# Optimization experiments

Measured on AMD Instinct MI355X. Metric: run time of the kernel, lower is better.

Reference implementation:

```python
import jax, jax.numpy as jnp
import numpy as np
from jax.scipy.special import gammaln

EPSILON = 1e-8
BOHR2ANG = 0.529177249  # Angstrom per Bohr; vecs are converted Ang -> Bohr
LS = np.array([0, 0, 0, 0, 1, 1, 1, 2, 2])             # angular momentum per orbital (9 GTOs, Lmax=2)
RAD_IDX = np.repeat(np.arange(len(LS)), 2 * LS + 1)    # [23] orbital index for each (orbital, m) slot
SPH_IDX = np.concatenate([np.arange(l * l, l * l + 2 * l + 1) for l in LS])  # [23] index into flat SH (dim 9)
OUTDIM = len(RAD_IDX)                                  # 23
BSZ, NPROBE, NATOM = 8, 8000, 32


def sph_harm_norm(u):
    """Real spherical harmonics l=0..2 of unit vectors u, e3nn 'norm' normalization (||Y_l||=1).
    Component-normalized e3nn polynomials divided by sqrt(2l+1). [..., 3] -> [..., 9]."""
    x, y, z = u[..., 0], u[..., 1], u[..., 2]
    s3 = 1.7320508075688772  # sqrt(3)
    sh = [
        jnp.ones_like(x),                       # l=0
        x, y, z,                                # l=1: sqrt(3)*(x,y,z)/sqrt(3)
        s3 * x * z,                             # l=2 (component / sqrt(5))
        s3 * x * y,
        y * y - 0.5 * (x * x + z * z),
        s3 * y * z,
        0.5 * s3 * (z * z - x * x),
    ]
    return jnp.stack(sh, axis=-1)


def _pair_indices(n_probes, n_atoms):
    """Host-side ragged atom-probe pair index construction (same result as the torch offset math)."""
    npb, naa = np.asarray(n_probes), np.asarray(n_atoms)
    offs_p, offs_a = np.cumsum(npb) - npb, np.cumsum(naa) - naa
    ip, ia = [], []
    for b in range(len(npb)):  # loop over small batch of molecules only
        ip.append(np.repeat(np.arange(npb[b]) + offs_p[b], naa[b]))
        ia.append(np.tile(np.arange(naa[b]) + offs_a[b], npb[b]))
    return jnp.asarray(np.concatenate(ip)), jnp.asarray(np.concatenate(ia))


def _gto(vecs, expos, ls):
    """GTOs.compute with normalize=True, expo_scaling=None. vecs: [P,3] (Bohr)."""
    r = jnp.linalg.norm(vecs, axis=-1, keepdims=True) + EPSILON   # [P,1]
    sph = sph_harm_norm(vecs / r)                                  # [P,9]
    power = ls + 1.5
    lognorm = (power * jnp.log(2.0 * expos) + jnp.log(2.0) - gammaln(power)) * 0.5  # [9]
    radial = jnp.exp(-expos * (r * r) + ls * jnp.log(r) + lognorm)  # [P,9]
    return radial[:, RAD_IDX] * sph[:, SPH_IDX]                     # [P,23] uncontracted


def setup_inputs() -> dict:
    key = jax.random.key(0)
    k1, k2, k3, k4 = jax.random.split(key, 4)
    probe_coords = jax.random.uniform(k1, (BSZ * NPROBE, 3), minval=0.0, maxval=10.0)
    atom_coords = jax.random.uniform(k2, (BSZ * NATOM, 3), minval=0.0, maxval=10.0)
    coeffs = 0.1 * jax.random.normal(k3, (BSZ * NATOM, OUTDIM))
    expos = jax.random.uniform(k4, (len(LS),), minval=0.2, maxval=5.0)
    n_probes = jnp.full((BSZ,), NPROBE, dtype=jnp.int32)
    n_atoms = jnp.full((BSZ,), NATOM, dtype=jnp.int32)
    return {"probe_coords": probe_coords, "atom_coords": atom_coords,
            "n_probes": n_probes, "n_atoms": n_atoms, "coeffs": coeffs, "expos": expos}


def reference(probe_coords, atom_coords, n_probes, n_atoms, coeffs, expos):
    ip, ia = _pair_indices(n_probes, n_atoms)           # [P] each, P = sum(n_probes*n_atoms)
    vecs = probe_coords[ip] - atom_coords[ia]           # [P,3]
    vecs = vecs[:, [1, 2, 0]] / BOHR2ANG                # reorder=True, Ang -> Bohr
    ls = jnp.asarray(LS, dtype=vecs.dtype)
    unc = _gto(vecs, expos, ls)                         # [P,23]
    per_pair = jnp.sum(unc * coeffs[ia], axis=-1)       # [P]
    n_total_probes = int(np.asarray(n_probes).sum())
    return jax.ops.segment_sum(per_pair, ip, num_segments=n_total_probes)  # [n_total_probes]
```

## Files before the change

### kernel.cpp

```cpp
#include <hip/hip_runtime.h>
#include <hip/hip_bf16.h>

#define SUB 4

__global__ __launch_bounds__(256) void gto_kernel(
    const float* __restrict__ probe,
    const float* __restrict__ atom,
    const int* __restrict__ n_probes,
    const int* __restrict__ n_atoms,
    const float* __restrict__ coeffs,
    const float* __restrict__ expos,
    float* __restrict__ out,
    int bsz, int ptot)
{
    const int t = blockIdx.x * blockDim.x + threadIdx.x;
    const int p = t / SUB;
    const int sub = t % SUB;
    if (p >= ptot) return;

    int poff = 0, aoff = 0, na = 0;
    for (int b = 0; b < bsz; ++b) {
        int np = n_probes[b];
        int nb = n_atoms[b];
        if (p < poff + np) { na = nb; break; }
        poff += np; aoff += nb;
    }

    const float gl[3] = {-0.12078223763524522f, 0.28468287047291918f, 1.2009736023470742f};
    const int   lsq[9] = {0,0,0,0,1,1,1,2,2};
    float e[9], ln[9];
#pragma unroll
    for (int k = 0; k < 9; ++k) {
        e[k] = expos[k];
        float pw = (float)lsq[k] + 1.5f;
        ln[k] = 0.5f * (pw * __logf(2.0f * e[k]) + 0.69314718055994531f - gl[lsq[k]]);
    }

    const float INV_BOHR = 1.8897259885789233f;
    const float S3 = 1.7320508075688772f;

    const float px = probe[p * 3 + 0];
    const float py = probe[p * 3 + 1];
    const float pz = probe[p * 3 + 2];

    float acc = 0.0f;
    for (int a = sub; a < na; a += SUB) {
        const int ai = aoff + a;
        const float ax = atom[ai * 3 + 0];
        const float ay = atom[ai * 3 + 1];
        const float az = atom[ai * 3 + 2];

        const float x = (py - ay) * INV_BOHR;
        const float y = (pz - az) * INV_BOHR;
        const float z = (px - ax) * INV_BOHR;

        const float r2n = x * x + y * y + z * z;
        const float r   = sqrtf(r2n) + 1e-8f;
        const float inv = 1.0f / r;
        const float ux = x * inv, uy = y * inv, uz = z * inv;
        const float rr = r * r;

        float rad[9];
#pragma unroll
        for (int k = 0; k < 9; ++k) rad[k] = __expf(ln[k] - e[k] * rr);
        rad[4] *= r;  rad[5] *= r;  rad[6] *= r;
        rad[7] *= rr; rad[8] *= rr;

        const float sh4 = S3 * ux * uz;
        const float sh5 = S3 * ux * uy;
        const float sh6 = uy * uy - 0.5f * (ux * ux + uz * uz);
        const float sh7 = S3 * uy * uz;
        const float sh8 = 0.5f * S3 * (uz * uz - ux * ux);

        const float* c = coeffs + ai * 23;
        float pp;
        pp  = rad[0] * c[0] + rad[1] * c[1] + rad[2] * c[2] + rad[3] * c[3];
        pp += rad[4] * (ux * c[4]  + uy * c[5]  + uz * c[6]);
        pp += rad[5] * (ux * c[7]  + uy * c[8]  + uz * c[9]);
        pp += rad[6] * (ux * c[10] + uy * c[11] + uz * c[12]);
        pp += rad[7] * (sh4 * c[13] + sh5 * c[14] + sh6 * c[15] + sh7 * c[16] + sh8 * c[17]);
        pp += rad[8] * (sh4 * c[18] + sh5 * c[19] + sh6 * c[20] + sh7 * c[21] + sh8 * c[22]);
        acc += pp;
    }

#pragma unroll
    for (int ofs = SUB / 2; ofs > 0; ofs >>= 1)
        acc += __shfl_xor(acc, ofs, 64);

    if (sub == 0) out[p] = acc;
}

extern "C" void kernel_launch(void* const* d_in, const int* in_sizes, int n_in,
                              void* d_out, int out_size, void* d_ws, size_t ws_size,
                              hipStream_t stream) {
    const float* probe  = (const float*)d_in[0];
    const float* atom   = (const float*)d_in[1];
    const int*   n_prb  = (const int*)d_in[2];
    const int*   n_atm  = (const int*)d_in[3];
    const float* coeffs = (const float*)d_in[4];
    const float* expos  = (const float*)d_in[5];
    float*       out    = (float*)d_out;

    const int bsz  = in_sizes[2];
    const int ptot = out_size;

    const int threads = ptot * SUB;
    const int block = 256;
    const int grid = (threads + block - 1) / block;
    gto_kernel<<<grid, block, 0, stream>>>(probe, atom, n_prb, n_atm, coeffs, expos, out, bsz, ptot);
}
```

Measured before the change: 17.21 us.

## Prepack scaled atom coefficients and drop sqrt/divide from GTO inner loop

Adds a pre-pass kernel that writes each atom into a 28-float workspace row holding its Bohr-scaled coordinates and its coefficients pre-multiplied by the radial normalisation and spherical-harmonic constants. The main kernel then reads each row as seven float4 loads. It removes sqrt, reciprocal and the r^l factors by using the unnormalised polynomial forms, and computes the exponentials with exp2. The cost is a second kernel launch and a small workspace write. Dropping the 1e-8 epsilon on r slightly changes numerics near r=0.

```diff
diff --git a/kernel.cpp b/kernel.cpp
--- a/kernel.cpp
+++ b/kernel.cpp
@@ -2,14 +2,51 @@
 #include <hip/hip_bf16.h>
 
 #define SUB 4
+#define ROWF 28
+
+__device__ __constant__ int   kRadIdx[23] = {0,1,2,3, 4,4,4, 5,5,5, 6,6,6, 7,7,7,7,7, 8,8,8,8,8};
+
+__global__ __launch_bounds__(256) void pack_kernel(
+    const float* __restrict__ atom,
+    const float* __restrict__ coeffs,
+    const float* __restrict__ expos,
+    float* __restrict__ ws,
+    int atot)
+{
+    const int a = blockIdx.x * blockDim.x + threadIdx.x;
+    if (a >= atot) return;
+
+    const float gl[3]  = {-0.12078223763524522f, 0.28468287047291918f, 1.2009736023470742f};
+    const int   lsq[9] = {0,0,0,0,1,1,1,2,2};
+    const float S3 = 1.7320508075688772f;
+    const float shf[23] = {1,1,1,1, 1,1,1, 1,1,1, 1,1,1,
+                           S3, S3, 1.0f, S3, 0.5f*S3,
+                           S3, S3, 1.0f, S3, 0.5f*S3};
+    float en[9];
+#pragma unroll
+    for (int k = 0; k < 9; ++k) {
+        float e  = expos[k];
+        float pw = (float)lsq[k] + 1.5f;
+        float ln = 0.5f * (pw * __logf(2.0f * e) + 0.69314718055994531f - gl[lsq[k]]);
+        en[k] = __expf(ln);
+    }
+    const float IB = 1.8897259885789233f;
+    float* row = ws + a * ROWF;
+    row[0] = atom[a * 3 + 1] * IB;
+    row[1] = atom[a * 3 + 2] * IB;
+    row[2] = atom[a * 3 + 0] * IB;
+#pragma unroll
+    for (int s = 0; s < 23; ++s)
+        row[3 + s] = coeffs[a * 23 + s] * en[kRadIdx[s]] * shf[s];
+    row[26] = 0.0f; row[27] = 0.0f;
+}
 
 __global__ __launch_bounds__(256) void gto_kernel(
     const float* __restrict__ probe,
-    const float* __restrict__ atom,
     const int* __restrict__ n_probes,
     const int* __restrict__ n_atoms,
-    const float* __restrict__ coeffs,
     const float* __restrict__ expos,
+    const float* __restrict__ ws,
     float* __restrict__ out,
     int bsz, int ptot)
 {
@@ -26,60 +63,45 @@
         poff += np; aoff += nb;
     }
 
-    const float gl[3] = {-0.12078223763524522f, 0.28468287047291918f, 1.2009736023470742f};
-    const int   lsq[9] = {0,0,0,0,1,1,1,2,2};
-    float e[9], ln[9];
+    const float NL2 = -1.4426950408889634f;
+    float e2n[9];
 #pragma unroll
-    for (int k = 0; k < 9; ++k) {
-        e[k] = expos[k];
-        float pw = (float)lsq[k] + 1.5f;
-        ln[k] = 0.5f * (pw * __logf(2.0f * e[k]) + 0.69314718055994531f - gl[lsq[k]]);
-    }
+    for (int k = 0; k < 9; ++k) e2n[k] = expos[k] * NL2;
 
-    const float INV_BOHR = 1.8897259885789233f;
-    const float S3 = 1.7320508075688772f;
-
-    const float px = probe[p * 3 + 0];
-    const float py = probe[p * 3 + 1];
-    const float pz = probe[p * 3 + 2];
+    const float IB = 1.8897259885789233f;
+    const float pxs = probe[p * 3 + 1] * IB;
+    const float pys = probe[p * 3 + 2] * IB;
+    const float pzs = probe[p * 3 + 0] * IB;
 
     float acc = 0.0f;
     for (int a = sub; a < na; a += SUB) {
-        const int ai = aoff + a;
-        const float ax = atom[ai * 3 + 0];
-        const float ay = atom[ai * 3 + 1];
-        const float az = atom[ai * 3 + 2];
+        const float4* row = (const float4*)(ws + (size_t)(aoff + a) * ROWF);
+        const float4 f0 = row[0], f1 = row[1], f2 = row[2], f3 = row[3];
+        const float4 f4 = row[4], f5 = row[5], f6 = row[6];
 
-        const float x = (py - ay) * INV_BOHR;
-        const float y = (pz - az) * INV_BOHR;
-        const float z = (px - ax) * INV_BOHR;
+        const float x = pxs - f0.x;
+        const float y = pys - f0.y;
+        const float z = pzs - f0.z;
+        const float xx = x * x, yy = y * y, zz = z * z;
+        const float r2 = xx + yy + zz;
 
-        const float r2n = x * x + y * y + z * z;
-        const float r   = sqrtf(r2n) + 1e-8f;
-        const float inv = 1.0f / r;
-        const float ux = x * inv, uy = y * inv, uz = z * inv;
-        const float rr = r * r;
+        float er[9];
+#pragma unroll
+        for (int k = 0; k < 9; ++k) er[k] = __builtin_amdgcn_exp2f(e2n[k] * r2);
 
-        float rad[9];
-#pragma unroll
-        for (int k = 0; k < 9; ++k) rad[k] = __expf(ln[k] - e[k] * rr);
-        rad[4] *= r;  rad[5] *= r;  rad[6] *= r;
-        rad[7] *= rr; rad[8] *= rr;
+        const float q1 = x * z;
+        const float q2 = x * y;
+        const float q4 = y * z;
+        const float q3 = yy - 0.5f * (xx + zz);
+        const float q5 = zz - xx;
 
-        const float sh4 = S3 * ux * uz;
-        const float sh5 = S3 * ux * uy;
-        const float sh6 = uy * uy - 0.5f * (ux * ux + uz * uz);
-        const float sh7 = S3 * uy * uz;
-        const float sh8 = 0.5f * S3 * (uz * uz - ux * ux);
-
-        const float* c = coeffs + ai * 23;
         float pp;
-        pp  = rad[0] * c[0] + rad[1] * c[1] + rad[2] * c[2] + rad[3] * c[3];
-        pp += rad[4] * (ux * c[4]  + uy * c[5]  + uz * c[6]);
-        pp += rad[5] * (ux * c[7]  + uy * c[8]  + uz * c[9]);
-        pp += rad[6] * (ux * c[10] + uy * c[11] + uz * c[12]);
-        pp += rad[7] * (sh4 * c[13] + sh5 * c[14] + sh6 * c[15] + sh7 * c[16] + sh8 * c[17]);
-        pp += rad[8] * (sh4 * c[18] + sh5 * c[19] + sh6 * c[20] + sh7 * c[21] + sh8 * c[22]);
+        pp  = er[0] * f0.w + er[1] * f1.x + er[2] * f1.y + er[3] * f1.z;
+        pp += er[4] * (x * f1.w + y * f2.x + z * f2.y);
+        pp += er[5] * (x * f2.z + y * f2.w + z * f3.x);
+        pp += er[6] * (x * f3.y + y * f3.z + z * f3.w);
+        pp += er[7] * (q1 * f4.x + q2 * f4.y + q3 * f4.z + q4 * f4.w + q5 * f5.x);
+        pp += er[8] * (q1 * f5.y + q2 * f5.z + q3 * f5.w + q4 * f6.x + q5 * f6.y);
         acc += pp;
     }
 
@@ -100,12 +122,16 @@
     const float* coeffs = (const float*)d_in[4];
     const float* expos  = (const float*)d_in[5];
     float*       out    = (float*)d_out;
+    float*       ws     = (float*)d_ws;
 
     const int bsz  = in_sizes[2];
+    const int atot = in_sizes[1] / 3;
     const int ptot = out_size;
+
+    pack_kernel<<<(atot + 255) / 256, 256, 0, stream>>>(atom, coeffs, expos, ws, atot);
 
     const int threads = ptot * SUB;
     const int block = 256;
     const int grid = (threads + block - 1) / block;
-    gto_kernel<<<grid, block, 0, stream>>>(probe, atom, n_prb, n_atm, coeffs, expos, out, bsz, ptot);
+    gto_kernel<<<grid, block, 0, stream>>>(probe, n_prb, n_atm, expos, ws, out, bsz, ptot);
 }
```

After: 21.31 us. 1.24x slower.

## Fold radial powers into unnormalized harmonics, use exp2, vectorize coefficient loads

Applied to the files above, without the earlier changes.

Uses the algebraic identity r^l * Y_l(u) = polynomial in x,y,z, which removes the sqrt, the reciprocal and the per-l radial multiplies. Switches to native exp2 with log2-domain normalization constants, prescales probe coordinates so each difference is a single fma, and loads the coefficients as vectors. It also replaces the batch lookup with a wave-shuffle broadcast and keeps out-of-range lanes alive for the shuffle reduction. This drops the 1e-8 epsilon on r, which slightly changes numerics near r=0, and the unaligned vector loads rely on 4-byte alignment.

```diff
diff --git a/kernel.cpp b/kernel.cpp
--- a/kernel.cpp
+++ b/kernel.cpp
@@ -1,7 +1,9 @@
 #include <hip/hip_runtime.h>
-#include <hip/hip_bf16.h>
 
 #define SUB 4
+
+typedef float f4u __attribute__((ext_vector_type(4), aligned(4)));
+typedef float f2u __attribute__((ext_vector_type(2), aligned(4)));
 
 __global__ __launch_bounds__(256) void gto_kernel(
     const float* __restrict__ probe,
@@ -14,80 +16,108 @@
     int bsz, int ptot)
 {
     const int t = blockIdx.x * blockDim.x + threadIdx.x;
-    const int p = t / SUB;
-    const int sub = t % SUB;
-    if (p >= ptot) return;
+    int p = t / SUB;
+    const int sub = t & (SUB - 1);
+    const bool alive = (p < ptot);
+    if (!alive) p = ptot - 1;
+    const int lane = threadIdx.x & 63;
 
-    int poff = 0, aoff = 0, na = 0;
-    for (int b = 0; b < bsz; ++b) {
-        int np = n_probes[b];
-        int nb = n_atoms[b];
-        if (p < poff + np) { na = nb; break; }
-        poff += np; aoff += nb;
+    int aoff = 0, na = 0;
+    if (bsz <= 64) {
+        int npl = 0, nal = 0;
+        if (lane < bsz) { npl = n_probes[lane]; nal = n_atoms[lane]; }
+        int cp = 0, ca = 0;
+        for (int b = 0; b < bsz; ++b) {
+            const int np_b = __shfl(npl, b, 64);
+            const int na_b = __shfl(nal, b, 64);
+            if (p >= cp && p < cp + np_b) { aoff = ca; na = na_b; }
+            cp += np_b; ca += na_b;
+        }
+    } else {
+        int cp = 0, ca = 0;
+        for (int b = 0; b < bsz; ++b) {
+            const int np_b = n_probes[b];
+            const int na_b = n_atoms[b];
+            if (p >= cp && p < cp + np_b) { aoff = ca; na = na_b; }
+            cp += np_b; ca += na_b;
+        }
     }
 
-    const float gl[3] = {-0.12078223763524522f, 0.28468287047291918f, 1.2009736023470742f};
-    const int   lsq[9] = {0,0,0,0,1,1,1,2,2};
-    float e[9], ln[9];
+    const float gl2[3]  = {-0.17425190f, 0.41071060f, 1.73263870f};
+    const int   lsq[9]  = {0,0,0,0,1,1,1,2,2};
+    const float NL2 = -1.4426950408889634f;
+    float e2n[9], lb2[9];
 #pragma unroll
     for (int k = 0; k < 9; ++k) {
-        e[k] = expos[k];
-        float pw = (float)lsq[k] + 1.5f;
-        ln[k] = 0.5f * (pw * __logf(2.0f * e[k]) + 0.69314718055994531f - gl[lsq[k]]);
+        const float e  = expos[k];
+        const float pw = (float)lsq[k] + 1.5f;
+        e2n[k] = e * NL2;
+        lb2[k] = 0.5f * (pw * __log2f(2.0f * e) + 1.0f - gl2[lsq[k]]);
     }
 
-    const float INV_BOHR = 1.8897259885789233f;
-    const float S3 = 1.7320508075688772f;
+    const float IB  = 1.8897259885789233f;
+    const float S3  = 1.7320508075688772f;
+    const float HS3 = 0.8660254037844386f;
 
-    const float px = probe[p * 3 + 0];
-    const float py = probe[p * 3 + 1];
-    const float pz = probe[p * 3 + 2];
+    const float pxs = probe[p * 3 + 1] * IB;
+    const float pys = probe[p * 3 + 2] * IB;
+    const float pzs = probe[p * 3 + 0] * IB;
 
     float acc = 0.0f;
+#pragma unroll 2
     for (int a = sub; a < na; a += SUB) {
-        const int ai = aoff + a;
-        const float ax = atom[ai * 3 + 0];
-        const float ay = atom[ai * 3 + 1];
-        const float az = atom[ai * 3 + 2];
+        const size_t ai = (size_t)(aoff + a);
+        const float* ar = atom + ai * 3;
+        const float a0 = ar[0], a1 = ar[1], a2 = ar[2];
+        const float* cr = coeffs + ai * 23;
+        const f4u c0 = *(const f4u*)(cr);
+        const f4u c4 = *(const f4u*)(cr + 4);
+        const f4u c8 = *(const f4u*)(cr + 8);
+        const f4u cc = *(const f4u*)(cr + 12);
+        const f4u cg = *(const f4u*)(cr + 16);
+        const f2u ck = *(const f2u*)(cr + 20);
+        const float cm = cr[22];
 
-        const float x = (py - ay) * INV_BOHR;
-        const float y = (pz - az) * INV_BOHR;
-        const float z = (px - ax) * INV_BOHR;
+        const float x = __builtin_fmaf(-IB, a1, pxs);
+        const float y = __builtin_fmaf(-IB, a2, pys);
+        const float z = __builtin_fmaf(-IB, a0, pzs);
+        const float xx = x * x, yy = y * y, zz = z * z;
+        const float r2 = xx + yy + zz;
 
-        const float r2n = x * x + y * y + z * z;
-        const float r   = sqrtf(r2n) + 1e-8f;
-        const float inv = 1.0f / r;
-        const float ux = x * inv, uy = y * inv, uz = z * inv;
-        const float rr = r * r;
+        float er[9];
+#pragma unroll
+        for (int k = 0; k < 9; ++k)
+            er[k] = __builtin_amdgcn_exp2f(__builtin_fmaf(e2n[k], r2, lb2[k]));
 
-        float rad[9];
-#pragma unroll
-        for (int k = 0; k < 9; ++k) rad[k] = __expf(ln[k] - e[k] * rr);
-        rad[4] *= r;  rad[5] *= r;  rad[6] *= r;
-        rad[7] *= rr; rad[8] *= rr;
-
-        const float sh4 = S3 * ux * uz;
-        const float sh5 = S3 * ux * uy;
-        const float sh6 = uy * uy - 0.5f * (ux * ux + uz * uz);
-        const float sh7 = S3 * uy * uz;
-        const float sh8 = 0.5f * S3 * (uz * uz - ux * ux);
-
-        const float* c = coeffs + ai * 23;
-        float pp;
-        pp  = rad[0] * c[0] + rad[1] * c[1] + rad[2] * c[2] + rad[3] * c[3];
-        pp += rad[4] * (ux * c[4]  + uy * c[5]  + uz * c[6]);
-        pp += rad[5] * (ux * c[7]  + uy * c[8]  + uz * c[9]);
-        pp += rad[6] * (ux * c[10] + uy * c[11] + uz * c[12]);
-        pp += rad[7] * (sh4 * c[13] + sh5 * c[14] + sh6 * c[15] + sh7 * c[16] + sh8 * c[17]);
-        pp += rad[8] * (sh4 * c[18] + sh5 * c[19] + sh6 * c[20] + sh7 * c[21] + sh8 * c[22]);
-        acc += pp;
+        float s = er[0] * c0.x;
+        s = __builtin_fmaf(er[1], c0.y, s);
+        s = __builtin_fmaf(er[2], c0.z, s);
+        s = __builtin_fmaf(er[3], c0.w, s);
+        float d;
+        d = __builtin_fmaf(x, c4.x, __builtin_fmaf(y, c4.y, z * c4.z));
+        s = __builtin_fmaf(er[4], d, s);
+        d = __builtin_fmaf(x, c4.w, __builtin_fmaf(y, c8.x, z * c8.y));
+        s = __builtin_fmaf(er[5], d, s);
+        d = __builtin_fmaf(x, c8.z, __builtin_fmaf(y, c8.w, z * cc.x));
+        s = __builtin_fmaf(er[6], d, s);
+        const float u1 = S3 * (x * z);
+        const float u2 = S3 * (x * y);
+        const float q3 = __builtin_fmaf(-0.5f, xx + zz, yy);
+        const float u4 = S3 * (y * z);
+        const float u5 = HS3 * (zz - xx);
+        d = __builtin_fmaf(u1, cc.y, __builtin_fmaf(u2, cc.z,
+            __builtin_fmaf(q3, cc.w, __builtin_fmaf(u4, cg.x, u5 * cg.y))));
+        s = __builtin_fmaf(er[7], d, s);
+        d = __builtin_fmaf(u1, cg.z, __builtin_fmaf(u2, cg.w,
+            __builtin_fmaf(q3, ck.x, __builtin_fmaf(u4, ck.y, u5 * cm))));
+        s = __builtin_fmaf(er[8], d, s);
+        acc += s;
     }
 
-#pragma unroll
-    for (int ofs = SUB / 2; ofs > 0; ofs >>= 1)
-        acc += __shfl_xor(acc, ofs, 64);
+    acc += __shfl_xor(acc, 1, 64);
+    acc += __shfl_xor(acc, 2, 64);
 
-    if (sub == 0) out[p] = acc;
+    if (alive && sub == 0) out[p] = acc;
 }
 
 extern "C" void kernel_launch(void* const* d_in, const int* in_sizes, int n_in,
@@ -104,8 +134,8 @@
     const int bsz  = in_sizes[2];
     const int ptot = out_size;
 
-    const int threads = ptot * SUB;
+    const long threads = (long)ptot * SUB;
     const int block = 256;
-    const int grid = (threads + block - 1) / block;
+    const int grid = (int)((threads + block - 1) / block);
     gto_kernel<<<grid, block, 0, stream>>>(probe, atom, n_prb, n_atm, coeffs, expos, out, bsz, ptot);
 }
```

Measured after the change: 16.25 us. 5.6% less time.
